# Optimization experiments

Hardware: AMD Instinct MI355X
Metric: run time of the kernel (lower is better)

Reference implementation:

```python
import jax, jax.numpy as jnp
import numpy as np
import math

N_HEAD = 16
ROPE_BASE = 10000.0


def _rope(x):
    # x: [B, S, H, Dh]
    S, d = x.shape[1], x.shape[-1]
    inv_freq = 1.0 / (ROPE_BASE ** (jnp.arange(0, d, 2, dtype=jnp.float32) / d))
    t = jnp.arange(S, dtype=jnp.float32)
    freqs = jnp.einsum('i,j->ij', t, inv_freq)              # [S, d/2]
    emb = jnp.concatenate([freqs, freqs], axis=-1)          # [S, d]
    cos = jnp.cos(emb)[None, :, None, :]
    sin = jnp.sin(emb)[None, :, None, :]
    x1, x2 = jnp.split(x, 2, axis=-1)
    x_rot = jnp.concatenate([-x2, x1], axis=-1)
    return x * cos + x_rot * sin


def setup_inputs() -> dict:
    key = jax.random.key(0)
    ks = jax.random.split(key, 6)
    B, S, D = 2, 2048, 1024
    x = jax.random.normal(ks[0], (B, S, D), dtype=jnp.float32)
    w = lambda k: jax.random.normal(k, (D, D), dtype=jnp.float32) * 0.02
    return {'x': x, 'wq': w(ks[1]), 'wk': w(ks[2]), 'wv': w(ks[3]),
            'wg': w(ks[4]), 'wo': w(ks[5])}


def reference(x, wq, wk, wv, wg, wo):
    B, S, D = x.shape
    H = N_HEAD
    Dh = D // H

    # projections (torch Linear: y = x @ W^T)
    q = (x @ wq.T).reshape(B, S, H, Dh)
    k = (x @ wk.T).reshape(B, S, H, Dh)
    v = (x @ wv.T).reshape(B, S, H, Dh)

    q = _rope(q)
    k = _rope(k)

    q = q.transpose(0, 2, 1, 3)  # [B,H,S,Dh]
    k = k.transpose(0, 2, 1, 3)
    v = v.transpose(0, 2, 1, 3)

    # per-head exponential decay mask (causal)
    idx = jnp.arange(S)
    d_mask = jnp.tril(idx[:, None] - idx[None, :]).astype(jnp.float32)  # [S,S]
    gamma = 1.0 - jnp.exp2(-5.0 - jnp.arange(H, dtype=jnp.float32))     # [H]
    causal = jnp.tril(jnp.ones((S, S), dtype=jnp.float32))
    decay_matrix = jnp.power(gamma[:, None, None], d_mask) * causal     # [H,S,S]

    retention = jnp.einsum('bhsd,bhtd->bhst', q, k) / math.sqrt(Dh)
    retention = retention * decay_matrix[None]                          # [B,H,S,S]

    out = jnp.einsum('bhst,bhtd->bhsd', retention, v)
    out = out.transpose(0, 2, 1, 3).reshape(B, S, D)

    g = jax.nn.silu(x @ wg.T)
    return (out * g) @ wo.T
```

## Files before the change

kernel.cpp:

```cpp
#include <hip/hip_runtime.h>
#include <hip/hip_bf16.h>

typedef unsigned short u16;
typedef unsigned int u32;
typedef __attribute__((ext_vector_type(8))) short short8;
typedef __attribute__((ext_vector_type(4))) float f32x4;

#define S_LEN 2048
#define D_DIM 1024
#define NH    16
#define DH    64
#define B_SZ  2
#define M_ROWS (B_SZ * S_LEN)
#define NCHUNK (S_LEN / 64)

__device__ __forceinline__ u16 f2bf(float f) {
  u32 u = __float_as_uint(f);
  u += 0x7FFFu + ((u >> 16) & 1u);
  return (u16)(u >> 16);
}
__device__ __forceinline__ float bf2f(u16 u) {
  return __uint_as_float(((u32)u) << 16);
}
__device__ __forceinline__ u32 pack_bf2(float lo, float hi) {
  __hip_bfloat162 p = __float22bfloat162_rn(make_float2(lo, hi));
  u32 r;
  __builtin_memcpy(&r, &p, 4);
  return r;
}

__device__ __forceinline__ void gll16(const void* g, void* l) {
  __builtin_amdgcn_global_load_lds((const __attribute__((address_space(1))) u32*)g,
                                   (__attribute__((address_space(3))) u32*)l,
                                   16, 0, 0);
}

#define SP1() __builtin_amdgcn_s_setprio(1)
#define SP0() __builtin_amdgcn_s_setprio(0)
#define BAR() __builtin_amdgcn_s_barrier()
#define LGKM0() do { asm volatile("s_waitcnt lgkmcnt(0)" ::: "memory"); \
                     __builtin_amdgcn_sched_barrier(0); } while (0)

__global__ __launch_bounds__(256) void prep_kernel(
    const float* __restrict__ x,
    const float* __restrict__ wq, const float* __restrict__ wk,
    const float* __restrict__ wv, const float* __restrict__ wg,
    const float* __restrict__ wo,
    u16* __restrict__ xb, u16* __restrict__ wcat, float2* __restrict__ rope)
{
  const int bid = blockIdx.x, tid = threadIdx.x;
  if (bid < 4096) {
    const int i = bid * 256 + tid;
    const float4 v = ((const float4*)x)[i];
    u32* d = (u32*)xb;
    d[2 * i]     = (u32)f2bf(v.x) | ((u32)f2bf(v.y) << 16);
    d[2 * i + 1] = (u32)f2bf(v.z) | ((u32)f2bf(v.w) << 16);
  } else if (bid < 9216) {
    const int t = bid - 4096;
    const int seg = t >> 10;
    const float* src = seg == 0 ? wq : seg == 1 ? wk : seg == 2 ? wv : seg == 3 ? wg : wo;
    const int i = (t & 1023) * 256 + tid;
    const float4 v = ((const float4*)src)[i];
    u32* d = (u32*)(wcat + (size_t)seg * D_DIM * D_DIM);
    d[2 * i]     = (u32)f2bf(v.x) | ((u32)f2bf(v.y) << 16);
    d[2 * i + 1] = (u32)f2bf(v.z) | ((u32)f2bf(v.w) << 16);
  } else {
    const int i = (bid - 9216) * 256 + tid;
    const int s = i >> 5, j = i & 31;
    float inv = exp2f(-(float)j * (13.287712379549449f / 32.f));
    float fr = (float)s * inv;
    rope[i] = make_float2(cosf(fr), sinf(fr));
  }
}

__global__ __launch_bounds__(512, 2) void proj_kernel(
    const u16* __restrict__ xb, const u16* __restrict__ wcat,
    u16* __restrict__ qb, u16* __restrict__ kb, u16* __restrict__ kT,
    u16* __restrict__ vT, u16* __restrict__ gb,
    const float2* __restrict__ rope)
{
  __shared__ u16 lds[65536];
  const int tid = threadIdx.x, lane = tid & 63, wid = tid >> 6;
  const int wm = wid >> 2, wn = wid & 3;
  const int l15 = lane & 15, l4 = lane >> 4;

  const int bid = blockIdx.x;
  const int sw = (bid & 7) * 32 + (bid >> 3);
  const int m0 = (sw & 15) * 256;
  const int n0 = (sw >> 4) * 256;

  f32x4 acc[8][4];
  #pragma unroll
  for (int m = 0; m < 8; ++m)
    #pragma unroll
    for (int n = 0; n < 4; ++n)
      acc[m][n] = (f32x4){0.f, 0.f, 0.f, 0.f};

  short8 a[4][2], b0[2][2], b1[2][2];

  auto stA = [&](int t, int h) {
    u16* dst = lds + ((t & 1) * 2 + h) * 8192;
    const u16* src = xb + (size_t)(m0 + h * 128) * D_DIM + t * 64;
    #pragma unroll
    for (int j = 0; j < 2; ++j) {
      const int c = tid + j * 512, row = c >> 3, ch = c & 7;
      gll16(src + (size_t)row * D_DIM + ((ch ^ (row & 7)) << 3), dst + c * 8);
    }
  };
  auto stB = [&](int t, int h) {
    u16* dst = lds + 32768 + ((t & 1) * 2 + h) * 8192;
    const u16* src = wcat + (size_t)(n0 + h * 128) * D_DIM + t * 64;
    #pragma unroll
    for (int j = 0; j < 2; ++j) {
      const int c = tid + j * 512, row = c >> 3, ch = c & 7;
      gll16(src + (size_t)row * D_DIM + ((ch ^ (row & 7)) << 3), dst + c * 8);
    }
  };
  auto ldA = [&](int d, int mh) {
    const u16* base = lds + (d * 2 + wm) * 8192;
    #pragma unroll
    for (int m = 0; m < 4; ++m) {
      const int lr = mh * 64 + m * 16 + l15;
      #pragma unroll
      for (int kk = 0; kk < 2; ++kk)
        a[m][kk] = *(const short8*)(base + lr * 64 + (((kk * 4 + l4) ^ (lr & 7)) << 3));
    }
  };
  auto ldB = [&](short8 (&b)[2][2], int d, int nh) {
    const u16* base = lds + 32768 + (d * 2 + (wn >> 1)) * 8192;
    #pragma unroll
    for (int j = 0; j < 2; ++j) {
      const int lr = (wn & 1) * 64 + (nh * 2 + j) * 16 + l15;
      #pragma unroll
      for (int kk = 0; kk < 2; ++kk)
        b[j][kk] = *(const short8*)(base + lr * 64 + (((kk * 4 + l4) ^ (lr & 7)) << 3));
    }
  };
  auto quad = [&](int mh, int nh, short8 (&b)[2][2]) {
    #pragma unroll
    for (int m = 0; m < 4; ++m)
      #pragma unroll
      for (int j = 0; j < 2; ++j)
        #pragma unroll
        for (int kk = 0; kk < 2; ++kk)
          acc[mh * 4 + m][nh * 2 + j] =
              __builtin_amdgcn_mfma_f32_16x16x32_bf16(a[m][kk], b[j][kk],
                                                      acc[mh * 4 + m][nh * 2 + j], 0, 0, 0);
  };

  stB(0, 0); stA(0, 0); stB(0, 1); stA(0, 1); stB(1, 0); stB(1, 1);
  asm volatile("s_waitcnt vmcnt(4)" ::: "memory");
  BAR();

  for (int i = 0; i < 8; ++i) {
    const int t1 = 2 * i + 1, t2 = 2 * i + 2, t3 = 2 * i + 3;
    ldA(0, 0); ldB(b0, 0, 0);
    stA(t1, 0);
    asm volatile("s_waitcnt lgkmcnt(8)" ::: "memory");
    BAR(); LGKM0();
    SP1(); quad(0, 0, b0); SP0();
    BAR();
    ldB(b1, 0, 1);
    stA(t1, 1);
    BAR(); LGKM0();
    SP1(); quad(0, 1, b1); SP0();
    BAR();
    ldA(0, 1);
    if (t2 < 16) stB(t2, 0);
    BAR(); LGKM0();
    SP1(); quad(1, 0, b0); SP0();
    BAR();
    if (t2 < 16) stA(t2, 0);
    BAR(); LGKM0();
    SP1(); quad(1, 1, b1); SP0();
    if (i == 7) asm volatile("s_waitcnt vmcnt(0)" ::: "memory");
    else        asm volatile("s_waitcnt vmcnt(4)" ::: "memory");
    BAR();
    ldA(1, 0); ldB(b0, 1, 0);
    if (t2 < 16) stB(t2, 1);
    asm volatile("s_waitcnt lgkmcnt(8)" ::: "memory");
    BAR(); LGKM0();
    SP1(); quad(0, 0, b0); SP0();
    BAR();
    ldB(b1, 1, 1);
    if (t2 < 16) stA(t2, 1);
    BAR(); LGKM0();
    SP1(); quad(0, 1, b1); SP0();
    BAR();
    ldA(1, 1);
    if (t3 < 16) stB(t3, 0);
    BAR(); LGKM0();
    SP1(); quad(1, 0, b0); SP0();
    BAR();
    if (t3 < 16) stB(t3, 1);
    BAR(); LGKM0();
    SP1(); quad(1, 1, b1); SP0();
    if (i < 7) asm volatile("s_waitcnt vmcnt(4)" ::: "memory");
    BAR();
  }

  const int gcol = n0 + wn * 64;
  const int z = gcol >> 10;
  const int hh = (gcol >> 6) & (NH - 1);
  const int mcol = gcol & (D_DIM - 1);
  const int rbase = m0 + wm * 128 + l4 * 4;
  const float lgh = log2f(1.f - exp2f(-5.f - (float)hh));

  if (z <= 1) {
    u16* dst = z ? kb : qb;
    const float slg  = z ? -lgh : lgh;
    const float base = z ? 1.f : 0.125f;
    #pragma unroll
    for (int m = 0; m < 8; ++m) {
      float o1v[2][4], o2v[2][4];
      #pragma unroll
      for (int r = 0; r < 4; ++r) {
        const int row = rbase + m * 16 + r;
        const int s = row & (S_LEN - 1);
        const float sc = base * exp2f((float)(s & 63) * slg);
        #pragma unroll
        for (int n = 0; n < 2; ++n) {
          const int dh0 = n * 16 + l15;
          const float2 cs = rope[s * 32 + dh0];
          const float x1 = acc[m][n][r], x2 = acc[m][n + 2][r];
          const float o1 = (x1 * cs.x - x2 * cs.y) * sc;
          const float o2 = (x2 * cs.x + x1 * cs.y) * sc;
          dst[(size_t)row * D_DIM + mcol + n * 16 + l15]       = f2bf(o1);
          dst[(size_t)row * D_DIM + mcol + (n + 2) * 16 + l15] = f2bf(o2);
          o1v[n][r] = o1; o2v[n][r] = o2;
        }
      }
      if (z == 1) {
        const int row0 = rbase + m * 16;
        const int bb = row0 >> 11, sr = row0 & (S_LEN - 1);
        #pragma unroll
        for (int n = 0; n < 2; ++n) {
          const int dh0 = n * 16 + l15;
          const uint2 p1 = make_uint2(pack_bf2(o1v[n][0], o1v[n][1]), pack_bf2(o1v[n][2], o1v[n][3]));
          const uint2 p2 = make_uint2(pack_bf2(o2v[n][0], o2v[n][1]), pack_bf2(o2v[n][2], o2v[n][3]));
          *(uint2*)(kT + (size_t)((bb * NH + hh) * DH + dh0) * S_LEN + sr)      = p1;
          *(uint2*)(kT + (size_t)((bb * NH + hh) * DH + dh0 + 32) * S_LEN + sr) = p2;
        }
      }
    }
  } else if (z == 2) {
    #pragma unroll
    for (int m = 0; m < 8; ++m) {
      const int row0 = rbase + m * 16;
      const int bb = row0 >> 11, sr = row0 & (S_LEN - 1);
      #pragma unroll
      for (int n = 0; n < 4; ++n) {
        const int dh = n * 16 + l15;
        const uint2 p = make_uint2(pack_bf2(acc[m][n][0], acc[m][n][1]),
                                   pack_bf2(acc[m][n][2], acc[m][n][3]));
        *(uint2*)(vT + (size_t)((bb * NH + hh) * DH + dh) * S_LEN + sr) = p;
      }
    }
  } else {
    #pragma unroll
    for (int m = 0; m < 8; ++m)
      #pragma unroll
      for (int n = 0; n < 4; ++n)
        #pragma unroll
        for (int r = 0; r < 4; ++r) {
          const int row = rbase + m * 16 + r;
          const float v = acc[m][n][r];
          gb[(size_t)row * D_DIM + mcol + n * 16 + l15] = f2bf(v / (1.f + __expf(-v)));
        }
  }
}

template<int BM, int BN, int WPM, int WPN>
__device__ __forceinline__ void gemm_bk32(const u16* __restrict__ A,
                                          const u16* __restrict__ W,
                                          const int m0, const int n0,
                                          u16* lds,
                                          f32x4 (&acc)[BM / (WPM * 16)][BN / (WPN * 16)])
{
  constexpr int T   = WPM * WPN * 64;
  constexpr int MR  = BM / (WPM * 16);
  constexpr int NR  = BN / (WPN * 16);
  constexpr int ALD = BM * 32;
  constexpr int BLD = BN * 32;
  constexpr int BUF = ALD + BLD;
  constexpr int NK  = D_DIM / 32;

  const int tid  = threadIdx.x;
  const int lane = tid & 63, wid = tid >> 6;
  const int wm = wid / WPN, wn = wid % WPN;
  const int l15 = lane & 15, l4 = lane >> 4;

  #pragma unroll
  for (int m = 0; m < MR; ++m)
    #pragma unroll
    for (int n = 0; n < NR; ++n)
      acc[m][n] = (f32x4){0.f, 0.f, 0.f, 0.f};

  auto stage = [&](int kt) {
    const int k0 = kt * 32;
    u16* la = lds + (kt & 3) * BUF;
    u16* lb = la + ALD;
    #pragma unroll
    for (int j = 0; j < BM * 4 / T; ++j) {
      const int c = tid + j * T;
      gll16(A + (size_t)(m0 + (c >> 2)) * D_DIM + k0 + (c & 3) * 8, la + c * 8);
    }
    #pragma unroll
    for (int j = 0; j < BN * 4 / T; ++j) {
      const int c = tid + j * T;
      gll16(W + (size_t)(n0 + (c >> 2)) * D_DIM + k0 + (c & 3) * 8, lb + c * 8);
    }
  };

  stage(0);
  stage(1);
  asm volatile("s_waitcnt vmcnt(4)" ::: "memory");
  BAR();
  __builtin_amdgcn_sched_barrier(0);

  for (int i = 0; i < NK; ++i) {
    if (i + 2 < NK) stage(i + 2);
    const u16* la = lds + (i & 3) * BUF + (wm * (BM / WPM) + l15) * 32 + l4 * 8;
    const u16* lb = lds + (i & 3) * BUF + ALD + (wn * (BN / WPN) + l15) * 32 + l4 * 8;
    short8 av[MR], bv[NR];
    #pragma unroll
    for (int m = 0; m < MR; ++m) av[m] = *(const short8*)(la + m * 16 * 32);
    #pragma unroll
    for (int n = 0; n < NR; ++n) bv[n] = *(const short8*)(lb + n * 16 * 32);
    SP1();
    #pragma unroll
    for (int m = 0; m < MR; ++m)
      #pragma unroll
      for (int n = 0; n < NR; ++n)
        acc[m][n] = __builtin_amdgcn_mfma_f32_16x16x32_bf16(av[m], bv[n], acc[m][n], 0, 0, 0);
    SP0();
    if (i + 2 < NK) asm volatile("s_waitcnt vmcnt(4)" ::: "memory");
    else            asm volatile("s_waitcnt vmcnt(0)" ::: "memory");
    BAR();
    __builtin_amdgcn_sched_barrier(0);
  }
}

__global__ __launch_bounds__(256) void chunk_accum(
    const u16* __restrict__ kT, const u16* __restrict__ vT,
    u16* __restrict__ At)
{
  const int tid = threadIdx.x, lane = tid & 63, w = tid >> 6;
  const int l15 = lane & 15, l4 = lane >> 4;
  const int bh = blockIdx.x >> 5, c = blockIdx.x & 31;

  short8 a[2], bfr[2][4];
  #pragma unroll
  for (int kk = 0; kk < 2; ++kk) {
    a[kk] = *(const short8*)(vT + (size_t)(bh * DH + w * 16 + l15) * S_LEN + c * 64 + kk * 32 + l4 * 8);
    #pragma unroll
    for (int n = 0; n < 4; ++n)
      bfr[kk][n] = *(const short8*)(kT + (size_t)(bh * DH + n * 16 + l15) * S_LEN + c * 64 + kk * 32 + l4 * 8);
  }
  f32x4 acc[4];
  #pragma unroll
  for (int n = 0; n < 4; ++n) acc[n] = (f32x4){0.f, 0.f, 0.f, 0.f};
  #pragma unroll
  for (int kk = 0; kk < 2; ++kk)
    #pragma unroll
    for (int n = 0; n < 4; ++n)
      acc[n] = __builtin_amdgcn_mfma_f32_16x16x32_bf16(a[kk], bfr[kk][n], acc[n], 0, 0, 0);

  u16* dst = At + ((size_t)(bh * NCHUNK + c)) * 4096;
  #pragma unroll
  for (int n = 0; n < 4; ++n)
    #pragma unroll
    for (int r = 0; r < 4; ++r)
      dst[(w * 16 + l4 * 4 + r) * 64 + n * 16 + l15] = f2bf(acc[n][r]);
}

__global__ __launch_bounds__(256) void chunk_scan(
    const u16* __restrict__ At, u16* __restrict__ St)
{
  const int gid = blockIdx.x * 256 + threadIdx.x;
  const int bh = gid >> 12, e = gid & 4095;
  const int h = bh & (NH - 1);
  const float lg = log2f(1.f - exp2f(-5.f - (float)h));
  const float gC = exp2f(64.f * lg);
  const u16* src = At + (size_t)bh * NCHUNK * 4096 + e;
  u16* dst = St + (size_t)bh * NCHUNK * 4096 + e;
  float s = 0.f;
  for (int c = 0; c < NCHUNK; ++c) {
    const float a = bf2f(src[(size_t)c * 4096]);
    dst[(size_t)c * 4096] = f2bf(s);
    s = gC * (s + a);
  }
}

__global__ __launch_bounds__(256) void chunk_out(
    const u16* __restrict__ qb, const u16* __restrict__ kb,
    const u16* __restrict__ vT, const u16* __restrict__ St,
    const u16* __restrict__ gb, u16* __restrict__ ob)
{
  __shared__ u16 Ps[4][16 * 64];

  const int tid = threadIdx.x, lane = tid & 63, w = tid >> 6;
  const int l15 = lane & 15, l4 = lane >> 4;
  const int bh = blockIdx.x >> 5, c = blockIdx.x & 31;
  const int b = bh >> 4, h = bh & (NH - 1);
  const int q0 = c * 64 + w * 16;

  short8 qfr[2], kf[2][4], vf[2][4], sf[2][4];
  #pragma unroll
  for (int kk = 0; kk < 2; ++kk) {
    qfr[kk] = *(const short8*)(qb + (size_t)(b * S_LEN + q0 + l15) * D_DIM + h * DH + kk * 32 + l4 * 8);
    #pragma unroll
    for (int t = 0; t < 4; ++t)
      kf[kk][t] = *(const short8*)(kb + (size_t)(b * S_LEN + c * 64 + t * 16 + l15) * D_DIM + h * DH + kk * 32 + l4 * 8);
    #pragma unroll
    for (int n = 0; n < 4; ++n) {
      vf[kk][n] = *(const short8*)(vT + (size_t)(bh * DH + n * 16 + l15) * S_LEN + c * 64 + kk * 32 + l4 * 8);
      sf[kk][n] = *(const short8*)(St + ((size_t)(bh * NCHUNK + c)) * 4096 + (n * 16 + l15) * 64 + kk * 32 + l4 * 8);
    }
  }

  f32x4 st[4];
  #pragma unroll
  for (int tf = 0; tf < 4; ++tf) st[tf] = (f32x4){0.f, 0.f, 0.f, 0.f};
  #pragma unroll
  for (int kk = 0; kk < 2; ++kk)
    #pragma unroll
    for (int tf = 0; tf < 4; ++tf)
      st[tf] = __builtin_amdgcn_mfma_f32_16x16x32_bf16(kf[kk][tf], qfr[kk], st[tf], 0, 0, 0);

  f32x4 acc[4];
  #pragma unroll
  for (int n = 0; n < 4; ++n) acc[n] = (f32x4){0.f, 0.f, 0.f, 0.f};
  #pragma unroll
  for (int kk = 0; kk < 2; ++kk)
    #pragma unroll
    for (int n = 0; n < 4; ++n)
      acc[n] = __builtin_amdgcn_mfma_f32_16x16x32_bf16(qfr[kk], sf[kk][n], acc[n], 0, 0, 0);

  u16* const psw = &Ps[w][0];
  const int qq = w * 16 + l15;
  #pragma unroll
  for (int tf = 0; tf < 4; ++tf) {
    const int tb = tf * 16 + l4 * 4;
    const float v0 = (tb + 0 <= qq) ? st[tf][0] : 0.f;
    const float v1 = (tb + 1 <= qq) ? st[tf][1] : 0.f;
    const float v2 = (tb + 2 <= qq) ? st[tf][2] : 0.f;
    const float v3 = (tb + 3 <= qq) ? st[tf][3] : 0.f;
    const uint2 u = make_uint2(pack_bf2(v0, v1), pack_bf2(v2, v3));
    const int boff = l15 * 128 + ((tf * 32 + l4 * 8) ^ ((l15 & 7) << 4));
    *(uint2*)((char*)psw + boff) = u;
  }

  #pragma unroll
  for (int kk = 0; kk < 2; ++kk) {
    const int boff = l15 * 128 + ((kk * 64 + l4 * 16) ^ ((l15 & 7) << 4));
    const short8 pa = *(const short8*)((const char*)psw + boff);
    #pragma unroll
    for (int n = 0; n < 4; ++n)
      acc[n] = __builtin_amdgcn_mfma_f32_16x16x32_bf16(pa, vf[kk][n], acc[n], 0, 0, 0);
  }

  #pragma unroll
  for (int n = 0; n < 4; ++n)
    #pragma unroll
    for (int r = 0; r < 4; ++r) {
      const size_t idx = (size_t)(b * S_LEN + q0 + l4 * 4 + r) * D_DIM + h * DH + n * 16 + l15;
      ob[idx] = f2bf(acc[n][r] * bf2f(gb[idx]));
    }
}

__global__ __launch_bounds__(256, 2) void final_kernel(
    const u16* __restrict__ ob, const u16* __restrict__ wob,
    float* __restrict__ out)
{
  __shared__ u16 lds[4 * (128 * 32 + 128 * 32)];
  f32x4 acc[4][4];
  const int bid = blockIdx.x;
  const int sw = (bid & 7) * 32 + (bid >> 3);
  const int n0 = (sw & 7) * 128;
  const int m0 = (sw >> 3) * 128;
  gemm_bk32<128, 128, 2, 2>(ob, wob, m0, n0, lds, acc);

  const int lane = threadIdx.x & 63, wid = threadIdx.x >> 6;
  const int wm = wid >> 1, wn = wid & 1;
  const int rbase = m0 + wm * 64 + (lane >> 4) * 4;
  const int cbase = n0 + wn * 64 + (lane & 15);
  #pragma unroll
  for (int m = 0; m < 4; ++m)
    #pragma unroll
    for (int n = 0; n < 4; ++n)
      #pragma unroll
      for (int r = 0; r < 4; ++r)
        out[(size_t)(rbase + m * 16 + r) * D_DIM + cbase + n * 16] = acc[m][n][r];
}

extern "C" void kernel_launch(void* const* d_in, const int* in_sizes, int n_in,
                              void* d_out, int out_size, void* d_ws, size_t ws_size,
                              hipStream_t stream) {
  (void)in_sizes; (void)n_in; (void)out_size; (void)ws_size;
  const float* x  = (const float*)d_in[0];
  const float* wq = (const float*)d_in[1];
  const float* wk = (const float*)d_in[2];
  const float* wv = (const float*)d_in[3];
  const float* wg = (const float*)d_in[4];
  const float* wo = (const float*)d_in[5];
  float* out = (float*)d_out;

  char* ws = (char*)d_ws;
  const size_t SZ_X = (size_t)M_ROWS * D_DIM * 2;
  const size_t SZ_W = (size_t)D_DIM * D_DIM * 2;
  u16* xb   = (u16*)(ws);
  u16* wcat = (u16*)(ws + SZ_X);
  u16* wob  = (u16*)(ws + SZ_X + 4 * SZ_W);
  u16* qb   = (u16*)(ws + 1 * SZ_X + 5 * SZ_W);
  u16* kb   = (u16*)(ws + 2 * SZ_X + 5 * SZ_W);
  u16* vT   = (u16*)(ws + 3 * SZ_X + 5 * SZ_W);
  u16* gb   = (u16*)(ws + 4 * SZ_X + 5 * SZ_W);
  u16* kT   = (u16*)(ws + 5 * SZ_X + 5 * SZ_W);
  u16* ob   = kT;
  float2* rope = (float2*)(ws + 6 * SZ_X + 5 * SZ_W);
  u16* St   = (u16*)(ws);
  u16* At   = (u16*)(ws + SZ_X);

  prep_kernel<<<dim3(9472), 256, 0, stream>>>(x, wq, wk, wv, wg, wo, xb, wcat, rope);

  proj_kernel<<<dim3(256), 512, 0, stream>>>(xb, wcat, qb, kb, kT, vT, gb, rope);

  chunk_accum<<<dim3(B_SZ * NH * NCHUNK), 256, 0, stream>>>(kT, vT, At);
  chunk_scan<<<dim3(B_SZ * NH * 4096 / 256), 256, 0, stream>>>(At, St);
  chunk_out<<<dim3(B_SZ * NH * NCHUNK), 256, 0, stream>>>(qb, kb, vT, St, gb, ob);

  final_kernel<<<dim3(256), 256, 0, stream>>>(ob, wob, out);
}
```

Before: 102.5 us.

## Store K/V transposes in chunk-tiled layout via LDS-staged swizzled writes

The projection epilogue now stages the K (after rope) and V transposes in shared memory with an XOR swizzle. It then writes them as contiguous 64x64 per-chunk tiles using 16-byte stores, replacing the scattered 8-byte strided global writes. chunk_accum and chunk_out read the new contiguous tile layout, which should give better coalesced loads. The cost is extra LDS traffic in the epilogue, and it relies on the main-loop LDS being free at that point without an explicit barrier.

```diff
diff --git a/kernel.cpp b/kernel.cpp
--- a/kernel.cpp
+++ b/kernel.cpp
@@ -75,8 +75,8 @@
 
 __global__ __launch_bounds__(512, 2) void proj_kernel(
     const u16* __restrict__ xb, const u16* __restrict__ wcat,
-    u16* __restrict__ qb, u16* __restrict__ kb, u16* __restrict__ kT,
-    u16* __restrict__ vT, u16* __restrict__ gb,
+    u16* __restrict__ qb, u16* __restrict__ kb, u16* __restrict__ kT2,
+    u16* __restrict__ vT2, u16* __restrict__ gb,
     const float2* __restrict__ rope)
 {
   __shared__ u16 lds[65536];
@@ -206,17 +206,22 @@
   const int rbase = m0 + wm * 128 + l4 * 4;
   const float lgh = log2f(1.f - exp2f(-5.f - (float)hh));
 
+  u16* const tw = lds + wid * 8192;
+  auto tput = [&](int dh, int s, float v) {
+    tw[dh * 128 + ((((s >> 3) ^ (dh & 15)) << 3) | (s & 7))] = f2bf(v);
+  };
+
   if (z <= 1) {
     u16* dst = z ? kb : qb;
     const float slg  = z ? -lgh : lgh;
     const float base = z ? 1.f : 0.125f;
     #pragma unroll
-    for (int m = 0; m < 8; ++m) {
-      float o1v[2][4], o2v[2][4];
+    for (int m = 0; m < 8; ++m)
       #pragma unroll
       for (int r = 0; r < 4; ++r) {
         const int row = rbase + m * 16 + r;
         const int s = row & (S_LEN - 1);
+        const int sloc = m * 16 + l4 * 4 + r;
         const float sc = base * exp2f((float)(s & 63) * slg);
         #pragma unroll
         for (int n = 0; n < 2; ++n) {
@@ -227,35 +232,17 @@
           const float o2 = (x2 * cs.x + x1 * cs.y) * sc;
           dst[(size_t)row * D_DIM + mcol + n * 16 + l15]       = f2bf(o1);
           dst[(size_t)row * D_DIM + mcol + (n + 2) * 16 + l15] = f2bf(o2);
-          o1v[n][r] = o1; o2v[n][r] = o2;
+          if (z == 1) { tput(dh0, sloc, o1); tput(dh0 + 32, sloc, o2); }
         }
       }
-      if (z == 1) {
-        const int row0 = rbase + m * 16;
-        const int bb = row0 >> 11, sr = row0 & (S_LEN - 1);
+  } else if (z == 2) {
+    #pragma unroll
+    for (int m = 0; m < 8; ++m)
+      #pragma unroll
+      for (int n = 0; n < 4; ++n)
         #pragma unroll
-        for (int n = 0; n < 2; ++n) {
-          const int dh0 = n * 16 + l15;
-          const uint2 p1 = make_uint2(pack_bf2(o1v[n][0], o1v[n][1]), pack_bf2(o1v[n][2], o1v[n][3]));
-          const uint2 p2 = make_uint2(pack_bf2(o2v[n][0], o2v[n][1]), pack_bf2(o2v[n][2], o2v[n][3]));
-          *(uint2*)(kT + (size_t)((bb * NH + hh) * DH + dh0) * S_LEN + sr)      = p1;
-          *(uint2*)(kT + (size_t)((bb * NH + hh) * DH + dh0 + 32) * S_LEN + sr) = p2;
-        }
-      }
-    }
-  } else if (z == 2) {
-    #pragma unroll
-    for (int m = 0; m < 8; ++m) {
-      const int row0 = rbase + m * 16;
-      const int bb = row0 >> 11, sr = row0 & (S_LEN - 1);
-      #pragma unroll
-      for (int n = 0; n < 4; ++n) {
-        const int dh = n * 16 + l15;
-        const uint2 p = make_uint2(pack_bf2(acc[m][n][0], acc[m][n][1]),
-                                   pack_bf2(acc[m][n][2], acc[m][n][3]));
-        *(uint2*)(vT + (size_t)((bb * NH + hh) * DH + dh) * S_LEN + sr) = p;
-      }
-    }
+        for (int r = 0; r < 4; ++r)
+          tput(n * 16 + l15, m * 16 + l4 * 4 + r, acc[m][n][r]);
   } else {
     #pragma unroll
     for (int m = 0; m < 8; ++m)
@@ -268,6 +255,22 @@
           gb[(size_t)row * D_DIM + mcol + n * 16 + l15] = f2bf(v / (1.f + __expf(-v)));
         }
   }
+
+  if (z == 1 || z == 2) {
+    const int row0 = m0 + wm * 128;
+    const int bb = row0 >> 11;
+    const int bh = bb * NH + hh;
+    const int c0 = (row0 & (S_LEN - 1)) >> 6;
+    u16* const dbase = (z == 1 ? kT2 : vT2);
+    const int dh4 = lane >> 4, scn = lane & 15;
+    #pragma unroll
+    for (int i = 0; i < 16; ++i) {
+      const int dh = i * 4 + dh4;
+      const short8 v = *(const short8*)(tw + dh * 128 + ((scn ^ (dh & 15)) << 3));
+      *(short8*)(dbase + ((size_t)((bh * NCHUNK + c0 + (scn >> 3)) * 64 + dh) * 64)
+                       + (scn & 7) * 8) = v;
+    }
+  }
 }
 
 template<int BM, int BN, int WPM, int WPN>
@@ -342,20 +345,21 @@
 }
 
 __global__ __launch_bounds__(256) void chunk_accum(
-    const u16* __restrict__ kT, const u16* __restrict__ vT,
+    const u16* __restrict__ kT2, const u16* __restrict__ vT2,
     u16* __restrict__ At)
 {
   const int tid = threadIdx.x, lane = tid & 63, w = tid >> 6;
   const int l15 = lane & 15, l4 = lane >> 4;
   const int bh = blockIdx.x >> 5, c = blockIdx.x & 31;
+  const size_t tbase = (size_t)(bh * NCHUNK + c) * 4096;
 
   short8 a[2], bfr[2][4];
   #pragma unroll
   for (int kk = 0; kk < 2; ++kk) {
-    a[kk] = *(const short8*)(vT + (size_t)(bh * DH + w * 16 + l15) * S_LEN + c * 64 + kk * 32 + l4 * 8);
+    a[kk] = *(const short8*)(vT2 + tbase + (w * 16 + l15) * 64 + kk * 32 + l4 * 8);
     #pragma unroll
     for (int n = 0; n < 4; ++n)
-      bfr[kk][n] = *(const short8*)(kT + (size_t)(bh * DH + n * 16 + l15) * S_LEN + c * 64 + kk * 32 + l4 * 8);
+      bfr[kk][n] = *(const short8*)(kT2 + tbase + (n * 16 + l15) * 64 + kk * 32 + l4 * 8);
   }
   f32x4 acc[4];
   #pragma unroll
@@ -366,7 +370,7 @@
     for (int n = 0; n < 4; ++n)
       acc[n] = __builtin_amdgcn_mfma_f32_16x16x32_bf16(a[kk], bfr[kk][n], acc[n], 0, 0, 0);
 
-  u16* dst = At + ((size_t)(bh * NCHUNK + c)) * 4096;
+  u16* dst = At + tbase;
   #pragma unroll
   for (int n = 0; n < 4; ++n)
     #pragma unroll
@@ -394,7 +398,7 @@
 
 __global__ __launch_bounds__(256) void chunk_out(
     const u16* __restrict__ qb, const u16* __restrict__ kb,
-    const u16* __restrict__ vT, const u16* __restrict__ St,
+    const u16* __restrict__ vT2, const u16* __restrict__ St,
     const u16* __restrict__ gb, u16* __restrict__ ob)
 {
   __shared__ u16 Ps[4][16 * 64];
@@ -404,6 +408,7 @@
   const int bh = blockIdx.x >> 5, c = blockIdx.x & 31;
   const int b = bh >> 4, h = bh & (NH - 1);
   const int q0 = c * 64 + w * 16;
+  const size_t tbase = (size_t)(bh * NCHUNK + c) * 4096;
 
   short8 qfr[2], kf[2][4], vf[2][4], sf[2][4];
   #pragma unroll
@@ -414,8 +419,8 @@
       kf[kk][t] = *(const short8*)(kb + (size_t)(b * S_LEN + c * 64 + t * 16 + l15) * D_DIM + h * DH + kk * 32 + l4 * 8);
     #pragma unroll
     for (int n = 0; n < 4; ++n) {
-      vf[kk][n] = *(const short8*)(vT + (size_t)(bh * DH + n * 16 + l15) * S_LEN + c * 64 + kk * 32 + l4 * 8);
-      sf[kk][n] = *(const short8*)(St + ((size_t)(bh * NCHUNK + c)) * 4096 + (n * 16 + l15) * 64 + kk * 32 + l4 * 8);
+      vf[kk][n] = *(const short8*)(vT2 + tbase + (n * 16 + l15) * 64 + kk * 32 + l4 * 8);
+      sf[kk][n] = *(const short8*)(St + tbase + (n * 16 + l15) * 64 + kk * 32 + l4 * 8);
     }
   }
 
@@ -514,21 +519,21 @@
   u16* wob  = (u16*)(ws + SZ_X + 4 * SZ_W);
   u16* qb   = (u16*)(ws + 1 * SZ_X + 5 * SZ_W);
   u16* kb   = (u16*)(ws + 2 * SZ_X + 5 * SZ_W);
-  u16* vT   = (u16*)(ws + 3 * SZ_X + 5 * SZ_W);
+  u16* vT2  = (u16*)(ws + 3 * SZ_X + 5 * SZ_W);
   u16* gb   = (u16*)(ws + 4 * SZ_X + 5 * SZ_W);
-  u16* kT   = (u16*)(ws + 5 * SZ_X + 5 * SZ_W);
-  u16* ob   = kT;
+  u16* kT2  = (u16*)(ws + 5 * SZ_X + 5 * SZ_W);
+  u16* ob   = kT2;
   float2* rope = (float2*)(ws + 6 * SZ_X + 5 * SZ_W);
   u16* St   = (u16*)(ws);
   u16* At   = (u16*)(ws + SZ_X);
 
   prep_kernel<<<dim3(9472), 256, 0, stream>>>(x, wq, wk, wv, wg, wo, xb, wcat, rope);
 
-  proj_kernel<<<dim3(256), 512, 0, stream>>>(xb, wcat, qb, kb, kT, vT, gb, rope);
-
-  chunk_accum<<<dim3(B_SZ * NH * NCHUNK), 256, 0, stream>>>(kT, vT, At);
+  proj_kernel<<<dim3(256), 512, 0, stream>>>(xb, wcat, qb, kb, kT2, vT2, gb, rope);
+
+  chunk_accum<<<dim3(B_SZ * NH * NCHUNK), 256, 0, stream>>>(kT2, vT2, At);
   chunk_scan<<<dim3(B_SZ * NH * 4096 / 256), 256, 0, stream>>>(At, St);
-  chunk_out<<<dim3(B_SZ * NH * NCHUNK), 256, 0, stream>>>(qb, kb, vT, St, gb, ob);
+  chunk_out<<<dim3(B_SZ * NH * NCHUNK), 256, 0, stream>>>(qb, kb, vT2, St, gb, ob);
 
   final_kernel<<<dim3(256), 256, 0, stream>>>(ob, wob, out);
 }
```

New measurement: 112.4 us. 1.1x slower.
